# Kernel optimization log

Hardware: AMD Instinct MI355X
Metric: run time of the kernel (lower is better)

## Reference

```python
import jax, jax.numpy as jnp
import numpy as np

N_NODES = 50000
C = 256          # in_channels == hidden_size
E = 800000


def setup_inputs() -> dict:
    key = jax.random.key(0)
    ks = jax.random.split(key, 12)
    x = jax.random.normal(ks[0], (N_NODES, C), dtype=jnp.float32)
    edge_index = jax.random.randint(ks[1], (2, E), 0, N_NODES, dtype=jnp.int64)
    edge_attr = jax.random.uniform(ks[2], (E,), dtype=jnp.float32)
    edge_weights_index = jax.random.randint(ks[3], (2, E), 0, N_NODES, dtype=jnp.int64)
    s = 1.0 / np.sqrt(C)
    # TopKPooling projection vector
    p_pool = jax.random.normal(ks[4], (C,), dtype=jnp.float32) * s
    # GRU (input=C, hidden=C): gates stacked [r, z, n]
    W_ih = jax.random.normal(ks[5], (3 * C, C), dtype=jnp.float32) * s
    W_hh = jax.random.normal(ks[6], (3 * C, C), dtype=jnp.float32) * s
    b_ih = jnp.zeros((3 * C,), dtype=jnp.float32)
    b_hh = jnp.zeros((3 * C,), dtype=jnp.float32)
    # initial evolving GCN weight [C, C]
    W_init = jax.random.normal(ks[7], (C, C), dtype=jnp.float32) * s
    # EdgeDecoder MLP
    lin1_w = jax.random.normal(ks[8], (C, 2 * C), dtype=jnp.float32) / np.sqrt(2 * C)
    lin1_b = jnp.zeros((C,), dtype=jnp.float32)
    lin2_w = jax.random.normal(ks[9], (1, C), dtype=jnp.float32) * s
    lin2_b = jnp.zeros((1,), dtype=jnp.float32)
    return {
        "x": x, "edge_index": edge_index, "edge_attr": edge_attr,
        "edge_weights_index": edge_weights_index,
        "p_pool": p_pool, "W_ih": W_ih, "W_hh": W_hh, "b_ih": b_ih, "b_hh": b_hh,
        "W_init": W_init, "lin1_w": lin1_w, "lin1_b": lin1_b,
        "lin2_w": lin2_w, "lin2_b": lin2_b,
    }


def _forward(x, edge_attr, p_pool, W_ih, W_hh, b_ih, b_hh, W_init,
             lin1_w, lin1_b, lin2_w, lin2_b, edge_index, edge_weights_index):
    n_nodes, c = x.shape
    # --- EvolveGCNH: TopK pooling summary (k = in_channels) ---
    score = x @ p_pool / jnp.linalg.norm(p_pool)          # [N]
    top_score, perm = jax.lax.top_k(score, c)             # [C]
    x_tilde = x[perm] * jnp.tanh(top_score)[:, None]      # [C, C]
    # --- GRU step: input x_tilde (batch=C), hidden = evolving weight W_init ---
    gi = x_tilde @ W_ih.T + b_ih                           # [C, 3C]
    gh = W_init @ W_hh.T + b_hh                            # [C, 3C]
    i_r, i_z, i_n = jnp.split(gi, 3, axis=1)
    h_r, h_z, h_n = jnp.split(gh, 3, axis=1)
    r = jax.nn.sigmoid(i_r + h_r)
    z = jax.nn.sigmoid(i_z + h_z)
    n = jnp.tanh(i_n + r * h_n)
    W = (1.0 - z) * n + z * W_init                         # [C, C] evolved GCN weight
    # --- GCNConv with fixed W, add_self_loops=False ---
    xw = x @ W                                             # [N, C]
    src, dst = edge_index[0], edge_index[1]
    deg = jax.ops.segment_sum(edge_attr, dst, num_segments=n_nodes)
    dinv = jnp.where(deg > 0, jax.lax.rsqrt(jnp.where(deg > 0, deg, 1.0)), 0.0)
    norm = dinv[src] * edge_attr * dinv[dst]               # [E]
    node_emb = jax.ops.segment_sum(xw[src] * norm[:, None], dst,
                                   num_segments=n_nodes)   # [N, C]
    # --- EdgeDecoder: gather src/trg, concat, MLP ---
    s_idx, t_idx = edge_weights_index[0], edge_weights_index[1]
    edge_emb = jnp.concatenate([node_emb[s_idx], node_emb[t_idx]], axis=1)  # [E, 2C]
    h = jax.nn.relu(edge_emb @ lin1_w.T + lin1_b)          # [E, C]
    pred = h @ lin2_w.T + lin2_b                           # [E, 1]
    return pred.reshape(-1)


def reference(x, edge_index, edge_attr, edge_weights_index, p_pool,
              W_ih, W_hh, b_ih, b_hh, W_init, lin1_w, lin1_b, lin2_w, lin2_b):
    # dropout is identity in eval mode
    return _forward(x, edge_attr, p_pool, W_ih, W_hh, b_ih, b_hh, W_init,
                    lin1_w, lin1_b, lin2_w, lin2_b, edge_index, edge_weights_index)
```

## Files before the change

### kernel.cpp

```cpp
#include <hip/hip_runtime.h>
#include <hip/hip_bf16.h>
#include <math.h>


typedef __attribute__((ext_vector_type(8))) short bf16x8;
typedef __attribute__((ext_vector_type(8))) unsigned short u16x8;
typedef __attribute__((ext_vector_type(4))) float f32x4;

#define WSHIFT 9
#define WMASK 511
#define NBUCK 98

__device__ __forceinline__ unsigned f2key(float f) {
  unsigned u = __float_as_uint(f);
  return (u & 0x80000000u) ? ~u : (u | 0x80000000u);
}

__device__ __forceinline__ unsigned short f2bf(float f) {
  unsigned u = __float_as_uint(f);
  unsigned r = u + 0x7fffu + ((u >> 16) & 1u);
  return (unsigned short)(r >> 16);
}
__device__ __forceinline__ float bf2f(unsigned short h) {
  return __uint_as_float((unsigned)h << 16);
}

template <int CTRL>
__device__ __forceinline__ float dpp_add(float s) {
  int t = __builtin_amdgcn_update_dpp(0, __float_as_int(s), CTRL, 0xf, 0xf, false);
  return s + __int_as_float(t);
}

__device__ __forceinline__ void gload16(const void* g, void* l) {
  __builtin_amdgcn_global_load_lds((const __attribute__((address_space(1))) void*)g,
                                   (__attribute__((address_space(3))) void*)l, 16, 0, 0);
}

__global__ void zero_kernel(float4* __restrict__ p, int n4) {
  int i = blockIdx.x * blockDim.x + threadIdx.x;
  if (i < n4) p[i] = make_float4(0.f, 0.f, 0.f, 0.f);
}

__global__ __launch_bounds__(256) void score_cast_kernel(const float* __restrict__ x,
                                                         const float* __restrict__ p,
                                                         float* __restrict__ score,
                                                         unsigned short* __restrict__ xh, int N) {
  int node = blockIdx.x * 4 + (threadIdx.x >> 6);
  int lane = threadIdx.x & 63;
  if (node >= N) return;
  float4 xv = ((const float4*)(x + (size_t)node * 256))[lane];
  ushort4 hv;
  hv.x = f2bf(xv.x);
  hv.y = f2bf(xv.y);
  hv.z = f2bf(xv.z);
  hv.w = f2bf(xv.w);
  ((ushort4*)(xh + (size_t)node * 256))[lane] = hv;
  float4 pv = ((const float4*)p)[lane];
  float s = xv.x * pv.x + xv.y * pv.y + xv.z * pv.z + xv.w * pv.w;
  float sp = pv.x * pv.x + pv.y * pv.y + pv.z * pv.z + pv.w * pv.w;
#pragma unroll
  for (int off = 32; off > 0; off >>= 1) {
    s += __shfl_down(s, off, 64);
    sp += __shfl_down(sp, off, 64);
  }
  if (lane == 0) score[node] = s / sqrtf(sp);
}

__global__ __launch_bounds__(256) void hist12_kernel(const float* __restrict__ score, int n,
                                                     int* __restrict__ gh) {
  __shared__ int lh[4096];
  int tid = threadIdx.x;
  for (int i = tid; i < 4096; i += 256) lh[i] = 0;
  __syncthreads();
  int idx = blockIdx.x * 256 + tid;
  int stride = gridDim.x * 256;
  for (int i = idx; i < n; i += stride) {
    unsigned key = f2key(score[i]);
    atomicAdd(&lh[key >> 20], 1);
  }
  __syncthreads();
  for (int i = tid; i < 4096; i += 256) {
    int v = lh[i];
    if (v) atomicAdd(&gh[i], v);
  }
}

__global__ __launch_bounds__(1024) void topk_kernel(const float* __restrict__ score, int n, int k,
                                                    const int* __restrict__ gh,
                                                    int* __restrict__ perm,
                                                    float* __restrict__ tts) {
  __shared__ int part[1024];
  __shared__ unsigned sT;
  int tid = threadIdx.x;
  {
    int b0 = tid * 4;
    int s0 = gh[b0], s1 = gh[b0 + 1], s2 = gh[b0 + 2], s3 = gh[b0 + 3];
    part[tid] = s0 + s1 + s2 + s3;
    __syncthreads();
    for (int off = 1; off < 1024; off <<= 1) {
      int v = part[tid];
      int add = (tid + off < 1024) ? part[tid + off] : 0;
      __syncthreads();
      part[tid] = v + add;
      __syncthreads();
    }
    int sufChunk = part[tid];
    int sufNext = (tid < 1023) ? part[tid + 1] : 0;
    if (sufNext < k && sufChunk >= k) {
      int run = sufNext;
      int b;
      run += s3;
      if (run >= k) b = b0 + 3;
      else {
        run += s2;
        if (run >= k) b = b0 + 2;
        else {
          run += s1;
          b = (run >= k) ? b0 + 1 : b0;
        }
      }
      sT = ((unsigned)b) << 20;
    }
  }
  __syncthreads();
  unsigned T = sT;
  __shared__ unsigned keys[1024];
  __shared__ int idxs[1024];
  __shared__ int cnt;
  if (tid == 0) cnt = 0;
  keys[tid] = 0u;
  idxs[tid] = 0x7fffffff;
  __syncthreads();
  for (int i = tid; i < n; i += 1024) {
    unsigned key = f2key(score[i]);
    if (key >= T) {
      int p = atomicAdd(&cnt, 1);
      if (p < 1024) { keys[p] = key; idxs[p] = i; }
    }
  }
  __syncthreads();
  for (int size = 2; size <= 1024; size <<= 1) {
    for (int stride = size >> 1; stride > 0; stride >>= 1) {
      int j = tid ^ stride;
      if (j > tid) {
        unsigned ka = keys[tid], kb = keys[j];
        int ia = idxs[tid], ib = idxs[j];
        bool aBefore = (ka > kb) || (ka == kb && ia < ib);
        bool up = ((tid & size) == 0);
        if (aBefore != up) {
          keys[tid] = kb; keys[j] = ka;
          idxs[tid] = ib; idxs[j] = ia;
        }
      }
      __syncthreads();
    }
  }
  if (tid < k) {
    int idx = idxs[tid];
    perm[tid] = idx;
    tts[tid] = tanhf(score[idx]);
  }
}

__global__ __launch_bounds__(256) void gru_kernel(const float* __restrict__ x,
                                                  const int* __restrict__ perm,
                                                  const float* __restrict__ tts,
                                                  const float* __restrict__ Wi,
                                                  const float* __restrict__ W_ih,
                                                  const float* __restrict__ W_hh,
                                                  const float* __restrict__ b_ih,
                                                  const float* __restrict__ b_hh,
                                                  unsigned short* __restrict__ WevoT) {
  int i = blockIdx.x, j = threadIdx.x;
  __shared__ float sx[256], sh[256];
  sx[j] = x[(size_t)perm[i] * 256 + j] * tts[i];
  sh[j] = Wi[i * 256 + j];
  __syncthreads();
  float gi[3], gh[3];
#pragma unroll
  for (int g = 0; g < 3; ++g) {
    int row = g * 256 + j;
    const float4* wi4 = (const float4*)(W_ih + (size_t)row * 256);
    const float4* wh4 = (const float4*)(W_hh + (size_t)row * 256);
    float si = 0.f, s2 = 0.f;
    for (int k4 = 0; k4 < 64; ++k4) {
      float4 wv = wi4[k4];
      float4 hv = wh4[k4];
      int k = k4 * 4;
      si += sx[k] * wv.x + sx[k + 1] * wv.y + sx[k + 2] * wv.z + sx[k + 3] * wv.w;
      s2 += sh[k] * hv.x + sh[k + 1] * hv.y + sh[k + 2] * hv.z + sh[k + 3] * hv.w;
    }
    gi[g] = si + b_ih[row];
    gh[g] = s2 + b_hh[row];
  }
  float r = 1.f / (1.f + expf(-(gi[0] + gh[0])));
  float z = 1.f / (1.f + expf(-(gi[1] + gh[1])));
  float nn = tanhf(gi[2] + r * gh[2]);
  float w = (1.f - z) * nn + z * sh[j];
  WevoT[(size_t)j * 256 + i] = f2bf(w);
}

__global__ __launch_bounds__(256) void lin1_cast_kernel(const float* __restrict__ lin1,
                                                        unsigned short* __restrict__ WAB) {
  int idx = blockIdx.x * 256 + threadIdx.x;
  int n = idx >> 9, k = idx & 511;
  unsigned short h = f2bf(lin1[idx]);
  if (k < 256)
    WAB[n * 256 + k] = h;
  else
    WAB[(256 + n) * 256 + (k - 256)] = h;
}

__global__ __launch_bounds__(512) void mfma_gemm128(const unsigned short* __restrict__ A,
                                                    const unsigned short* __restrict__ BT,
                                                    unsigned short* __restrict__ C1,
                                                    unsigned short* __restrict__ C2,
                                                    int M) {
  __shared__ unsigned short sA[128 * 32];
  __shared__ unsigned short sB[256 * 32];
  int tid = threadIdx.x;
  int wave = tid >> 6, lane = tid & 63;
  int quad = lane >> 4, r16 = lane & 15;
  int wm = wave >> 2, wn = wave & 3;
  int mbase = blockIdx.x * 128;
  const unsigned short* Bt = BT + ((size_t)blockIdx.y << 16);
  unsigned short* Cout = blockIdx.y ? C2 : C1;

  int srow = tid >> 2, scolq = tid & 3;
  const unsigned short* gA = A + (size_t)(mbase + srow) * 256 + scolq * 8;
  const unsigned short* gB0 = Bt + (size_t)srow * 256 + scolq * 8;
  const unsigned short* gB1 = Bt + (size_t)(128 + srow) * 256 + scolq * 8;
  unsigned short* lA = sA + wave * 512;
  unsigned short* lB0 = sB + wave * 512;
  unsigned short* lB1 = sB + 4096 + wave * 512;

  f32x4 acc[4][4];
#pragma unroll
  for (int i = 0; i < 4; ++i)
#pragma unroll
    for (int j = 0; j < 4; ++j) acc[i][j] = (f32x4){0.f, 0.f, 0.f, 0.f};

  const unsigned short* pA = sA + (wm * 64 + r16) * 32 + quad * 8;
  const unsigned short* pB = sB + (wn * 64 + r16) * 32 + quad * 8;

  for (int k0 = 0; k0 < 256; k0 += 32) {
    if (k0) __syncthreads();
    gload16(gA + k0, lA);
    gload16(gB0 + k0, lB0);
    gload16(gB1 + k0, lB1);
    __syncthreads();
    bf16x8 af[4], bfr[4];
#pragma unroll
    for (int mt = 0; mt < 4; ++mt) af[mt] = *(const bf16x8*)(pA + mt * 512);
#pragma unroll
    for (int nt = 0; nt < 4; ++nt) bfr[nt] = *(const bf16x8*)(pB + nt * 512);
#pragma unroll
    for (int mt = 0; mt < 4; ++mt)
#pragma unroll
      for (int nt = 0; nt < 4; ++nt)
        acc[mt][nt] = __builtin_amdgcn_mfma_f32_16x16x32_bf16(af[mt], bfr[nt], acc[mt][nt], 0, 0, 0);
  }
#pragma unroll
  for (int mt = 0; mt < 4; ++mt) {
#pragma unroll
    for (int rr = 0; rr < 4; ++rr) {
      int grow = mbase + wm * 64 + mt * 16 + quad * 4 + rr;
      if (grow < M) {
#pragma unroll
        for (int nt = 0; nt < 4; ++nt)
          Cout[(size_t)grow * 256 + wn * 64 + nt * 16 + r16] = f2bf(acc[mt][nt][rr]);
      }
    }
  }
}


__global__ __launch_bounds__(256) void bucket_hist_kernel(const int* __restrict__ ei,
                                                          const int* __restrict__ ewi,
                                                          int* __restrict__ bcnt1,
                                                          int* __restrict__ bcnt2, int E) {
  __shared__ int c1[128], c2[128];
  int tid = threadIdx.x;
  if (tid < 128) { c1[tid] = 0; c2[tid] = 0; }
  __syncthreads();
  int idx = blockIdx.x * 256 + tid;
  int stride = gridDim.x * 256;
  for (int e = idx; e < E; e += stride) {
    atomicAdd(&c1[ei[E + e] >> WSHIFT], 1);
    atomicAdd(&c2[ewi[e] >> WSHIFT], 1);
  }
  __syncthreads();
  if (tid < 128) {
    if (c1[tid]) atomicAdd(&bcnt1[tid], c1[tid]);
    if (c2[tid]) atomicAdd(&bcnt2[tid], c2[tid]);
  }
}

__global__ __launch_bounds__(128) void bucket_scan_kernel(const int* __restrict__ bcnt1,
                                                          const int* __restrict__ bcnt2,
                                                          int* __restrict__ bbase1,
                                                          int* __restrict__ bbase2,
                                                          int* __restrict__ gcur1,
                                                          int* __restrict__ gcur2,
                                                          int* __restrict__ rowp1,
                                                          int* __restrict__ rowp2, int N, int E) {
  __shared__ int ss[128];
  int tid = threadIdx.x;
  int v = (tid < NBUCK) ? bcnt1[tid] : 0;
  ss[tid] = v;
  __syncthreads();
  for (int off = 1; off < 128; off <<= 1) {
    int a = ss[tid];
    int b = (tid >= off) ? ss[tid - off] : 0;
    __syncthreads();
    ss[tid] = a + b;
    __syncthreads();
  }
  int excl = ss[tid] - v;
  if (tid < NBUCK) { bbase1[tid] = excl; gcur1[tid] = excl; }
  if (tid == NBUCK - 1) bbase1[NBUCK] = excl + v;
  __syncthreads();
  v = (tid < NBUCK) ? bcnt2[tid] : 0;
  ss[tid] = v;
  __syncthreads();
  for (int off = 1; off < 128; off <<= 1) {
    int a = ss[tid];
    int b = (tid >= off) ? ss[tid - off] : 0;
    __syncthreads();
    ss[tid] = a + b;
    __syncthreads();
  }
  excl = ss[tid] - v;
  if (tid < NBUCK) { bbase2[tid] = excl; gcur2[tid] = excl; }
  if (tid == NBUCK - 1) bbase2[NBUCK] = excl + v;
  if (tid == 0) { rowp1[N] = E; rowp2[N] = E; }
}

__global__ __launch_bounds__(256) void p1_conv_kernel(const int* __restrict__ ei,
                                                      const float* __restrict__ attr,
                                                      int* __restrict__ gcur,
                                                      int2* __restrict__ stage, int E) {
  __shared__ int cnt[128], cur[128];
  int tid = threadIdx.x;
  int base = blockIdx.x * 4096;
  if (tid < 128) cnt[tid] = 0;
  __syncthreads();
  int bk[16];
  int2 pl[16];
#pragma unroll
  for (int i = 0; i < 16; ++i) {
    int e = base + i * 256 + tid;
    bk[i] = -1;
    if (e < E) {
      int d = ei[E + e];
      int s = ei[e];
      bk[i] = d >> WSHIFT;
      pl[i] = make_int2(s | ((d & WMASK) << 16), __float_as_int(attr[e]));
      atomicAdd(&cnt[bk[i]], 1);
    }
  }
  __syncthreads();
  if (tid < NBUCK) {
    int c = cnt[tid];
    cur[tid] = c ? atomicAdd(&gcur[tid], c) : 0;
  }
  __syncthreads();
#pragma unroll
  for (int i = 0; i < 16; ++i) {
    if (bk[i] >= 0) {
      int pos = atomicAdd(&cur[bk[i]], 1);
      stage[pos] = pl[i];
    }
  }
}

__global__ __launch_bounds__(256) void p1_dec_kernel(const int* __restrict__ ewi,
                                                     int* __restrict__ gcur,
                                                     int2* __restrict__ stage, int E) {
  __shared__ int cnt[128], cur[128];
  int tid = threadIdx.x;
  int base = blockIdx.x * 4096;
  if (tid < 128) cnt[tid] = 0;
  __syncthreads();
  int bk[16];
  int2 pl[16];
#pragma unroll
  for (int i = 0; i < 16; ++i) {
    int e = base + i * 256 + tid;
    bk[i] = -1;
    if (e < E) {
      int s = ewi[e];
      int d = ewi[E + e];
      bk[i] = s >> WSHIFT;
      pl[i] = make_int2(d | ((s & WMASK) << 16), e);
      atomicAdd(&cnt[bk[i]], 1);
    }
  }
  __syncthreads();
  if (tid < NBUCK) {
    int c = cnt[tid];
    cur[tid] = c ? atomicAdd(&gcur[tid], c) : 0;
  }
  __syncthreads();
#pragma unroll
  for (int i = 0; i < 16; ++i) {
    if (bk[i] >= 0) {
      int pos = atomicAdd(&cur[bk[i]], 1);
      stage[pos] = pl[i];
    }
  }
}

__global__ __launch_bounds__(256) void p2_kernel(const int2* __restrict__ stage1,
                                                 const int* __restrict__ bbase1,
                                                 int2* __restrict__ esv,
                                                 int* __restrict__ rowp1,
                                                 float* __restrict__ dinv,
                                                 const int2* __restrict__ stage2,
                                                 const int* __restrict__ bbase2,
                                                 int2* __restrict__ eto,
                                                 int* __restrict__ rowp2, int N) {
  __shared__ int cnt[512];
  __shared__ float degs[512];
  __shared__ int pref[512];
  __shared__ int ss[256];
  int tid = threadIdx.x;
  bool isConv = blockIdx.x < NBUCK;
  int b = isConv ? blockIdx.x : blockIdx.x - NBUCK;
  const int2* stage = isConv ? stage1 : stage2;
  const int* bbase = isConv ? bbase1 : bbase2;
  int beg = bbase[b], end = bbase[b + 1];
  int node0 = b << WSHIFT;
  cnt[tid] = 0; cnt[tid + 256] = 0;
  degs[tid] = 0.f; degs[tid + 256] = 0.f;
  __syncthreads();
  for (int j = beg + tid; j < end; j += 256) {
    int2 p = stage[j];
    int loc = p.x >> 16;
    atomicAdd(&cnt[loc], 1);
    if (isConv) atomicAdd(&degs[loc], __int_as_float(p.y));
  }
  __syncthreads();
  int c0 = cnt[2 * tid], c1 = cnt[2 * tid + 1];
  ss[tid] = c0 + c1;
  __syncthreads();
  for (int off = 1; off < 256; off <<= 1) {
    int a = ss[tid];
    int bb = (tid >= off) ? ss[tid - off] : 0;
    __syncthreads();
    ss[tid] = a + bb;
    __syncthreads();
  }
  int excl = (tid ? ss[tid - 1] : 0);
  pref[2 * tid] = excl;
  pref[2 * tid + 1] = excl + c0;
  __syncthreads();
#pragma unroll
  for (int h = 0; h < 2; ++h) {
    int i = tid + h * 256;
    int node = node0 + i;
    if (node < N) {
      if (isConv) {
        rowp1[node] = beg + pref[i];
        float d = degs[i];
        dinv[node] = d > 0.f ? 1.f / sqrtf(d) : 0.f;
      } else {
        rowp2[node] = beg + pref[i];
      }
    }
  }
  __syncthreads();
  int2* outb = isConv ? esv : eto;
  for (int j = beg + tid; j < end; j += 256) {
    int2 p = stage[j];
    int loc = p.x >> 16;
    int pos = beg + atomicAdd(&pref[loc], 1);
    outb[pos] = make_int2(p.x & 0xFFFF, p.y);
  }
}

__global__ __launch_bounds__(256) void esv_scale_kernel(int4* __restrict__ esv,
                                                        const float* __restrict__ dinv, int E2) {
  int i = blockIdx.x * 256 + threadIdx.x;
  if (i < E2) {
    int4 p = esv[i];
    p.y = __float_as_int(__int_as_float(p.y) * dinv[p.x]);
    p.w = __float_as_int(__int_as_float(p.w) * dinv[p.z]);
    esv[i] = p;
  }
}

__global__ __launch_bounds__(256) void gcn_gather(const unsigned short* __restrict__ xw,
                                                  const int* __restrict__ row_ptr,
                                                  const int2* __restrict__ esv,
                                                  const float* __restrict__ dinv,
                                                  unsigned short* __restrict__ ne, int N) {
  int node = blockIdx.x * 4 + (threadIdx.x >> 6);
  int lane = threadIdx.x & 63;
  int g = lane & 15, q = lane >> 4;
  if (node >= N) return;
  int beg = row_ptr[node], end = row_ptr[node + 1];
  float acc[16];
#pragma unroll
  for (int c = 0; c < 16; ++c) acc[c] = 0.f;
  const unsigned short* xb = xw + g * 16;

  for (int cb = beg; cb < end; cb += 64) {
    int cend = cb + 64 < end ? cb + 64 : end;
    int me = cb + lane;
    int2 mm = (me < cend) ? esv[me] : make_int2(0, 0);
    int mx = mm.x;
    float mv = __int_as_float(mm.y);

    float vA = 0.f, vB = 0.f, vC = 0.f;
    u16x8 rAa, rAb, rBa, rBb, rCa, rCb;
    {
      int e = cb + q;
      int sx = __shfl(mx, q, 64);
      float tv = __shfl(mv, q, 64);
      vA = (e < cend) ? tv : 0.f;
      rAa = *(const u16x8*)(xb + (size_t)sx * 256);
      rAb = *(const u16x8*)(xb + (size_t)sx * 256 + 8);
    }
    if (cb + 4 < cend) {
      int e = cb + 4 + q;
      int sx = __shfl(mx, 4 + q, 64);
      float tv = __shfl(mv, 4 + q, 64);
      vB = (e < cend) ? tv : 0.f;
      rBa = *(const u16x8*)(xb + (size_t)sx * 256);
      rBb = *(const u16x8*)(xb + (size_t)sx * 256 + 8);
    } else { rBa = rAa; rBb = rAb; }
    if (cb + 8 < cend) {
      int e = cb + 8 + q;
      int sx = __shfl(mx, 8 + q, 64);
      float tv = __shfl(mv, 8 + q, 64);
      vC = (e < cend) ? tv : 0.f;
      rCa = *(const u16x8*)(xb + (size_t)sx * 256);
      rCb = *(const u16x8*)(xb + (size_t)sx * 256 + 8);
    } else { rCa = rAa; rCb = rAb; }

    for (int jb = cb; jb < cend; jb += 12) {
#pragma unroll
      for (int c = 0; c < 8; ++c) acc[c] += bf2f(rAa[c]) * vA;
#pragma unroll
      for (int c = 0; c < 8; ++c) acc[8 + c] += bf2f(rAb[c]) * vA;
      vA = 0.f;
      if (jb + 12 < cend) {
        int e = jb + 12 + q;
        int idx = (e - cb) & 63;
        int sx = __shfl(mx, idx, 64);
        float tv = __shfl(mv, idx, 64);
        vA = (e < cend) ? tv : 0.f;
        rAa = *(const u16x8*)(xb + (size_t)sx * 256);
        rAb = *(const u16x8*)(xb + (size_t)sx * 256 + 8);
      }
#pragma unroll
      for (int c = 0; c < 8; ++c) acc[c] += bf2f(rBa[c]) * vB;
#pragma unroll
      for (int c = 0; c < 8; ++c) acc[8 + c] += bf2f(rBb[c]) * vB;
      vB = 0.f;
      if (jb + 16 < cend) {
        int e = jb + 16 + q;
        int idx = (e - cb) & 63;
        int sx = __shfl(mx, idx, 64);
        float tv = __shfl(mv, idx, 64);
        vB = (e < cend) ? tv : 0.f;
        rBa = *(const u16x8*)(xb + (size_t)sx * 256);
        rBb = *(const u16x8*)(xb + (size_t)sx * 256 + 8);
      }
#pragma unroll
      for (int c = 0; c < 8; ++c) acc[c] += bf2f(rCa[c]) * vC;
#pragma unroll
      for (int c = 0; c < 8; ++c) acc[8 + c] += bf2f(rCb[c]) * vC;
      vC = 0.f;
      if (jb + 20 < cend) {
        int e = jb + 20 + q;
        int idx = (e - cb) & 63;
        int sx = __shfl(mx, idx, 64);
        float tv = __shfl(mv, idx, 64);
        vC = (e < cend) ? tv : 0.f;
        rCa = *(const u16x8*)(xb + (size_t)sx * 256);
        rCb = *(const u16x8*)(xb + (size_t)sx * 256 + 8);
      }
    }
  }
#pragma unroll
  for (int c = 0; c < 16; ++c) {
    acc[c] += __shfl_xor(acc[c], 16, 64);
    acc[c] += __shfl_xor(acc[c], 32, 64);
  }
  if (q == 0) {
    float dd = dinv[node];
    u16x8 o0, o1;
#pragma unroll
    for (int c = 0; c < 8; ++c) {
      o0[c] = f2bf(acc[c] * dd);
      o1[c] = f2bf(acc[8 + c] * dd);
    }
    *(u16x8*)(ne + (size_t)node * 256 + g * 16) = o0;
    *(u16x8*)(ne + (size_t)node * 256 + g * 16 + 8) = o1;
  }
}

__global__ __launch_bounds__(256) void edge_decode_csr(const unsigned short* __restrict__ A,
                                                       const unsigned short* __restrict__ Bm,
                                                       const int* __restrict__ row_ptr,
                                                       const int2* __restrict__ eto,
                                                       const float* __restrict__ b1,
                                                       const float* __restrict__ w2,
                                                       const float* __restrict__ b2,
                                                       float* __restrict__ out, int N) {
  int node = blockIdx.x * 4 + (threadIdx.x >> 6);
  int lane = threadIdx.x & 63;
  int g = lane & 15, q = lane >> 4;
  if (node >= N) return;
  int beg = row_ptr[node], end = row_ptr[node + 1];
  if (beg >= end) return;
  float a[16], w[16];
  {
    u16x8 a0 = *(const u16x8*)(A + (size_t)node * 256 + g * 16);
    u16x8 a1 = *(const u16x8*)(A + (size_t)node * 256 + g * 16 + 8);
    const float4* bp = (const float4*)(b1 + g * 16);
    const float4* wp = (const float4*)(w2 + g * 16);
#pragma unroll
    for (int i = 0; i < 4; ++i) {
      float4 bv = bp[i];
      float4 wv = wp[i];
      a[i * 4 + 0] = (i < 2 ? bf2f(a0[i * 4 + 0]) : bf2f(a1[i * 4 - 8])) + bv.x;
      a[i * 4 + 1] = (i < 2 ? bf2f(a0[i * 4 + 1]) : bf2f(a1[i * 4 - 7])) + bv.y;
      a[i * 4 + 2] = (i < 2 ? bf2f(a0[i * 4 + 2]) : bf2f(a1[i * 4 - 6])) + bv.z;
      a[i * 4 + 3] = (i < 2 ? bf2f(a0[i * 4 + 3]) : bf2f(a1[i * 4 - 5])) + bv.w;
      w[i * 4 + 0] = wv.x;
      w[i * 4 + 1] = wv.y;
      w[i * 4 + 2] = wv.z;
      w[i * 4 + 3] = wv.w;
    }
  }
  float base = b2[0];
  const unsigned short* Bb = Bm + g * 16;

  for (int cb = beg; cb < end; cb += 64) {
    int cend = cb + 64 < end ? cb + 64 : end;
    int me = cb + lane;
    int2 mm = (me < cend) ? eto[me] : make_int2(0, 0);
    int mx = mm.x, my = mm.y;

    bool okA = false, okB = false;
    int oA = 0, oB = 0;
    u16x8 rAa, rAb, rBa, rBb;
    {
      int e = cb + q;
      int sx = __shfl(mx, q, 64);
      oA = __shfl(my, q, 64);
      okA = e < cend;
      rAa = *(const u16x8*)(Bb + (size_t)sx * 256);
      rAb = *(const u16x8*)(Bb + (size_t)sx * 256 + 8);
    }
    if (cb + 4 < cend) {
      int e = cb + 4 + q;
      int sx = __shfl(mx, 4 + q, 64);
      oB = __shfl(my, 4 + q, 64);
      okB = e < cend;
      rBa = *(const u16x8*)(Bb + (size_t)sx * 256);
      rBb = *(const u16x8*)(Bb + (size_t)sx * 256 + 8);
    } else { rBa = rAa; rBb = rAb; }

    for (int jb = cb; jb < cend; jb += 8) {
      {
        float s0 = 0.f, s1 = 0.f;
#pragma unroll
        for (int c = 0; c < 8; ++c) s0 += fmaxf(a[c] + bf2f(rAa[c]), 0.f) * w[c];
#pragma unroll
        for (int c = 0; c < 8; ++c) s1 += fmaxf(a[8 + c] + bf2f(rAb[c]), 0.f) * w[8 + c];
        float s = s0 + s1;
        s = dpp_add<0x128>(s);
        s = dpp_add<0x124>(s);
        s = dpp_add<0x122>(s);
        s = dpp_add<0x121>(s);
        if (g == 0 && okA) out[oA] = s + base;
      }
      okA = false;
      if (jb + 8 < cend) {
        int e = jb + 8 + q;
        int idx = (e - cb) & 63;
        int sx = __shfl(mx, idx, 64);
        oA = __shfl(my, idx, 64);
        okA = e < cend;
        rAa = *(const u16x8*)(Bb + (size_t)sx * 256);
        rAb = *(const u16x8*)(Bb + (size_t)sx * 256 + 8);
      }
      {
        float s0 = 0.f, s1 = 0.f;
#pragma unroll
        for (int c = 0; c < 8; ++c) s0 += fmaxf(a[c] + bf2f(rBa[c]), 0.f) * w[c];
#pragma unroll
        for (int c = 0; c < 8; ++c) s1 += fmaxf(a[8 + c] + bf2f(rBb[c]), 0.f) * w[8 + c];
        float s = s0 + s1;
        s = dpp_add<0x128>(s);
        s = dpp_add<0x124>(s);
        s = dpp_add<0x122>(s);
        s = dpp_add<0x121>(s);
        if (g == 0 && okB) out[oB] = s + base;
      }
      okB = false;
      if (jb + 12 < cend) {
        int e = jb + 12 + q;
        int idx = (e - cb) & 63;
        int sx = __shfl(mx, idx, 64);
        oB = __shfl(my, idx, 64);
        okB = e < cend;
        rBa = *(const u16x8*)(Bb + (size_t)sx * 256);
        rBb = *(const u16x8*)(Bb + (size_t)sx * 256 + 8);
      }
    }
  }
}

extern "C" void kernel_launch(void* const* d_in, const int* in_sizes, int n_in,
                              void* d_out, int out_size, void* d_ws, size_t ws_size,
                              hipStream_t stream) {
  const float* x      = (const float*)d_in[0];
  const int*   ei     = (const int*)d_in[1];
  const float* attr   = (const float*)d_in[2];
  const int*   ewi    = (const int*)d_in[3];
  const float* p_pool = (const float*)d_in[4];
  const float* W_ih   = (const float*)d_in[5];
  const float* W_hh   = (const float*)d_in[6];
  const float* b_ih   = (const float*)d_in[7];
  const float* b_hh   = (const float*)d_in[8];
  const float* W_init = (const float*)d_in[9];
  const float* lin1_w = (const float*)d_in[10];
  const float* lin1_b = (const float*)d_in[11];
  const float* lin2_w = (const float*)d_in[12];
  const float* lin2_b = (const float*)d_in[13];
  float* out = (float*)d_out;

  const int C = 256;
  const int N = in_sizes[0] / C;
  const int E = in_sizes[2];

  char* ws = (char*)d_ws;
  size_t off = 0;
  auto alloc = [&](size_t bytes) {
    size_t o = off;
    off = (off + bytes + 255) & ~(size_t)255;
    return o;
  };
  float*          score  = (float*)(ws + alloc((size_t)N * 4));
  int*            perm   = (int*)(ws + alloc(C * 4));
  float*          tts    = (float*)(ws + alloc(C * 4));
  unsigned short* WevoT  = (unsigned short*)(ws + alloc((size_t)C * C * 2));
  unsigned short* WAB    = (unsigned short*)(ws + alloc((size_t)2 * C * C * 2));
  int   zeroInts = 4096 + 128 + 128;
  char* zbase    = ws + alloc((size_t)zeroInts * 4);
  int* ghist = (int*)zbase;
  int* bcnt1 = (int*)(zbase + 4096 * 4);
  int* bcnt2 = (int*)(zbase + 4096 * 4 + 128 * 4);
  int*            bbase1 = (int*)(ws + alloc((NBUCK + 1) * 4));
  int*            bbase2 = (int*)(ws + alloc((NBUCK + 1) * 4));
  int*            gcur1  = (int*)(ws + alloc(128 * 4));
  int*            gcur2  = (int*)(ws + alloc(128 * 4));
  float*          dinv   = (float*)(ws + alloc((size_t)N * 4));
  int*            rowp1  = (int*)(ws + alloc((size_t)(N + 1) * 4));
  int*            rowp2  = (int*)(ws + alloc((size_t)(N + 1) * 4));
  int2*           stage1 = (int2*)(ws + alloc((size_t)E * 8));
  int2*           stage2 = (int2*)(ws + alloc((size_t)E * 8));
  int2*           esv    = (int2*)(ws + alloc((size_t)E * 8));
  int2*           eto    = (int2*)(ws + alloc((size_t)E * 8));
  unsigned short* xh     = (unsigned short*)(ws + alloc((size_t)N * C * 2));
  unsigned short* xwh    = (unsigned short*)(ws + alloc((size_t)N * C * 2));
  unsigned short* Bbf    = (unsigned short*)(ws + alloc((size_t)N * C * 2));
  unsigned short* ne  = xh;
  unsigned short* Abf = xwh;

  zero_kernel<<<(zeroInts / 4 + 255) / 256, 256, 0, stream>>>((float4*)zbase, zeroInts / 4);

  score_cast_kernel<<<(N + 3) / 4, 256, 0, stream>>>(x, p_pool, score, xh, N);

  hist12_kernel<<<64, 256, 0, stream>>>(score, N, ghist);
  topk_kernel<<<1, 1024, 0, stream>>>(score, N, C, ghist, perm, tts);

  gru_kernel<<<C, C, 0, stream>>>(x, perm, tts, W_init, W_ih, W_hh, b_ih, b_hh, WevoT);

  mfma_gemm128<<<dim3((N + 127) / 128, 1), 512, 0, stream>>>(xh, WevoT, xwh, xwh, N);

  bucket_hist_kernel<<<256, 256, 0, stream>>>(ei, ewi, bcnt1, bcnt2, E);
  bucket_scan_kernel<<<1, 128, 0, stream>>>(bcnt1, bcnt2, bbase1, bbase2, gcur1, gcur2,
                                            rowp1, rowp2, N, E);
  p1_conv_kernel<<<(E + 4095) / 4096, 256, 0, stream>>>(ei, attr, gcur1, stage1, E);
  p1_dec_kernel<<<(E + 4095) / 4096, 256, 0, stream>>>(ewi, gcur2, stage2, E);
  p2_kernel<<<2 * NBUCK, 256, 0, stream>>>(stage1, bbase1, esv, rowp1, dinv,
                                           stage2, bbase2, eto, rowp2, N);

  esv_scale_kernel<<<(E / 2 + 255) / 256, 256, 0, stream>>>((int4*)esv, dinv, E / 2);

  gcn_gather<<<(N + 3) / 4, 256, 0, stream>>>(xwh, rowp1, esv, dinv, ne, N);

  lin1_cast_kernel<<<(2 * C * C) / 256, 256, 0, stream>>>(lin1_w, WAB);
  mfma_gemm128<<<dim3((N + 127) / 128, 2), 512, 0, stream>>>(ne, WAB, Abf, Bbf, N);

  edge_decode_csr<<<(N + 3) / 4, 256, 0, stream>>>(Abf, Bbf, rowp2, eto,
                                                   lin1_b, lin2_w, lin2_b, out, N);
}
```

Before: 466.9 us.

## Merge small kernels and deepen edge-decode prefetch pipeline to three stages

Folds the zeroing and lin1 bf16 cast into one init kernel, builds the score histogram with global atomics inside the score kernel, and merges the two bucket-partition kernels into one launch. It also drops the separate esv scaling pass by applying dinv[src] inside the GCN gather. The edge decoder now keeps three gather buffers in flight instead of two. The goal is fewer launches and more memory-level parallelism, at the cost of 50k global atomics on a small histogram and more registers in the decoder.

```diff
diff --git a/kernel.cpp b/kernel.cpp
--- a/kernel.cpp
+++ b/kernel.cpp
@@ -36,15 +36,29 @@
                                    (__attribute__((address_space(3))) void*)l, 16, 0, 0);
 }
 
-__global__ void zero_kernel(float4* __restrict__ p, int n4) {
-  int i = blockIdx.x * blockDim.x + threadIdx.x;
-  if (i < n4) p[i] = make_float4(0.f, 0.f, 0.f, 0.f);
+__global__ __launch_bounds__(256) void init_kernel(const float* __restrict__ lin1,
+                                                   unsigned short* __restrict__ WAB,
+                                                   int4* __restrict__ zb, int nz4) {
+  int b = blockIdx.x, tid = threadIdx.x;
+  if (b < 512) {
+    int idx = b * 256 + tid;
+    int n = idx >> 9, k = idx & 511;
+    unsigned short h = f2bf(lin1[idx]);
+    if (k < 256)
+      WAB[n * 256 + k] = h;
+    else
+      WAB[(256 + n) * 256 + (k - 256)] = h;
+  } else {
+    int j = (b - 512) * 256 + tid;
+    if (j < nz4) zb[j] = make_int4(0, 0, 0, 0);
+  }
 }
 
 __global__ __launch_bounds__(256) void score_cast_kernel(const float* __restrict__ x,
                                                          const float* __restrict__ p,
                                                          float* __restrict__ score,
-                                                         unsigned short* __restrict__ xh, int N) {
+                                                         unsigned short* __restrict__ xh,
+                                                         int* __restrict__ gh, int N) {
   int node = blockIdx.x * 4 + (threadIdx.x >> 6);
   int lane = threadIdx.x & 63;
   if (node >= N) return;
@@ -63,25 +77,10 @@
     s += __shfl_down(s, off, 64);
     sp += __shfl_down(sp, off, 64);
   }
-  if (lane == 0) score[node] = s / sqrtf(sp);
-}
-
-__global__ __launch_bounds__(256) void hist12_kernel(const float* __restrict__ score, int n,
-                                                     int* __restrict__ gh) {
-  __shared__ int lh[4096];
-  int tid = threadIdx.x;
-  for (int i = tid; i < 4096; i += 256) lh[i] = 0;
-  __syncthreads();
-  int idx = blockIdx.x * 256 + tid;
-  int stride = gridDim.x * 256;
-  for (int i = idx; i < n; i += stride) {
-    unsigned key = f2key(score[i]);
-    atomicAdd(&lh[key >> 20], 1);
-  }
-  __syncthreads();
-  for (int i = tid; i < 4096; i += 256) {
-    int v = lh[i];
-    if (v) atomicAdd(&gh[i], v);
+  if (lane == 0) {
+    float sc = s / sqrtf(sp);
+    score[node] = sc;
+    atomicAdd(&gh[f2key(sc) >> 20], 1);
   }
 }
 
@@ -200,17 +199,6 @@
   WevoT[(size_t)j * 256 + i] = f2bf(w);
 }
 
-__global__ __launch_bounds__(256) void lin1_cast_kernel(const float* __restrict__ lin1,
-                                                        unsigned short* __restrict__ WAB) {
-  int idx = blockIdx.x * 256 + threadIdx.x;
-  int n = idx >> 9, k = idx & 511;
-  unsigned short h = f2bf(lin1[idx]);
-  if (k < 256)
-    WAB[n * 256 + k] = h;
-  else
-    WAB[(256 + n) * 256 + (k - 256)] = h;
-}
-
 __global__ __launch_bounds__(512) void mfma_gemm128(const unsigned short* __restrict__ A,
                                                     const unsigned short* __restrict__ BT,
                                                     unsigned short* __restrict__ C1,
@@ -336,13 +324,20 @@
   if (tid == 0) { rowp1[N] = E; rowp2[N] = E; }
 }
 
-__global__ __launch_bounds__(256) void p1_conv_kernel(const int* __restrict__ ei,
+__global__ __launch_bounds__(256) void p1_both_kernel(const int* __restrict__ ei,
                                                       const float* __restrict__ attr,
-                                                      int* __restrict__ gcur,
-                                                      int2* __restrict__ stage, int E) {
+                                                      int* __restrict__ gcur1,
+                                                      int2* __restrict__ stage1,
+                                                      const int* __restrict__ ewi,
+                                                      int* __restrict__ gcur2,
+                                                      int2* __restrict__ stage2,
+                                                      int E, int nb) {
   __shared__ int cnt[128], cur[128];
   int tid = threadIdx.x;
-  int base = blockIdx.x * 4096;
+  bool conv = blockIdx.x < nb;
+  int base = (conv ? blockIdx.x : blockIdx.x - nb) * 4096;
+  int* gcur = conv ? gcur1 : gcur2;
+  int2* stage = conv ? stage1 : stage2;
   if (tid < 128) cnt[tid] = 0;
   __syncthreads();
   int bk[16];
@@ -352,47 +347,17 @@
     int e = base + i * 256 + tid;
     bk[i] = -1;
     if (e < E) {
-      int d = ei[E + e];
-      int s = ei[e];
-      bk[i] = d >> WSHIFT;
-      pl[i] = make_int2(s | ((d & WMASK) << 16), __float_as_int(attr[e]));
-      atomicAdd(&cnt[bk[i]], 1);
-    }
-  }
-  __syncthreads();
-  if (tid < NBUCK) {
-    int c = cnt[tid];
-    cur[tid] = c ? atomicAdd(&gcur[tid], c) : 0;
-  }
-  __syncthreads();
-#pragma unroll
-  for (int i = 0; i < 16; ++i) {
-    if (bk[i] >= 0) {
-      int pos = atomicAdd(&cur[bk[i]], 1);
-      stage[pos] = pl[i];
-    }
-  }
-}
-
-__global__ __launch_bounds__(256) void p1_dec_kernel(const int* __restrict__ ewi,
-                                                     int* __restrict__ gcur,
-                                                     int2* __restrict__ stage, int E) {
-  __shared__ int cnt[128], cur[128];
-  int tid = threadIdx.x;
-  int base = blockIdx.x * 4096;
-  if (tid < 128) cnt[tid] = 0;
-  __syncthreads();
-  int bk[16];
-  int2 pl[16];
-#pragma unroll
-  for (int i = 0; i < 16; ++i) {
-    int e = base + i * 256 + tid;
-    bk[i] = -1;
-    if (e < E) {
-      int s = ewi[e];
-      int d = ewi[E + e];
-      bk[i] = s >> WSHIFT;
-      pl[i] = make_int2(d | ((s & WMASK) << 16), e);
+      if (conv) {
+        int d = ei[E + e];
+        int s = ei[e];
+        bk[i] = d >> WSHIFT;
+        pl[i] = make_int2(s | ((d & WMASK) << 16), __float_as_int(attr[e]));
+      } else {
+        int s = ewi[e];
+        int d = ewi[E + e];
+        bk[i] = s >> WSHIFT;
+        pl[i] = make_int2(d | ((s & WMASK) << 16), e);
+      }
       atomicAdd(&cnt[bk[i]], 1);
     }
   }
@@ -479,17 +444,6 @@
   }
 }
 
-__global__ __launch_bounds__(256) void esv_scale_kernel(int4* __restrict__ esv,
-                                                        const float* __restrict__ dinv, int E2) {
-  int i = blockIdx.x * 256 + threadIdx.x;
-  if (i < E2) {
-    int4 p = esv[i];
-    p.y = __float_as_int(__int_as_float(p.y) * dinv[p.x]);
-    p.w = __float_as_int(__int_as_float(p.w) * dinv[p.z]);
-    esv[i] = p;
-  }
-}
-
 __global__ __launch_bounds__(256) void gcn_gather(const unsigned short* __restrict__ xw,
                                                   const int* __restrict__ row_ptr,
                                                   const int2* __restrict__ esv,
@@ -510,7 +464,7 @@
     int me = cb + lane;
     int2 mm = (me < cend) ? esv[me] : make_int2(0, 0);
     int mx = mm.x;
-    float mv = __int_as_float(mm.y);
+    float mv = __int_as_float(mm.y) * dinv[mx];
 
     float vA = 0.f, vB = 0.f, vC = 0.f;
     u16x8 rAa, rAb, rBa, rBb, rCa, rCb;
@@ -645,9 +599,9 @@
     int2 mm = (me < cend) ? eto[me] : make_int2(0, 0);
     int mx = mm.x, my = mm.y;
 
-    bool okA = false, okB = false;
-    int oA = 0, oB = 0;
-    u16x8 rAa, rAb, rBa, rBb;
+    bool okA = false, okB = false, okC = false;
+    int oA = 0, oB = 0, oC = 0;
+    u16x8 rAa, rAb, rBa, rBb, rCa, rCb;
     {
       int e = cb + q;
       int sx = __shfl(mx, q, 64);
@@ -664,8 +618,16 @@
       rBa = *(const u16x8*)(Bb + (size_t)sx * 256);
       rBb = *(const u16x8*)(Bb + (size_t)sx * 256 + 8);
     } else { rBa = rAa; rBb = rAb; }
-
-    for (int jb = cb; jb < cend; jb += 8) {
+    if (cb + 8 < cend) {
+      int e = cb + 8 + q;
+      int sx = __shfl(mx, 8 + q, 64);
+      oC = __shfl(my, 8 + q, 64);
+      okC = e < cend;
+      rCa = *(const u16x8*)(Bb + (size_t)sx * 256);
+      rCb = *(const u16x8*)(Bb + (size_t)sx * 256 + 8);
+    } else { rCa = rAa; rCb = rAb; }
+
+    for (int jb = cb; jb < cend; jb += 12) {
       {
         float s0 = 0.f, s1 = 0.f;
 #pragma unroll
@@ -680,8 +642,8 @@
         if (g == 0 && okA) out[oA] = s + base;
       }
       okA = false;
-      if (jb + 8 < cend) {
-        int e = jb + 8 + q;
+      if (jb + 12 < cend) {
+        int e = jb + 12 + q;
         int idx = (e - cb) & 63;
         int sx = __shfl(mx, idx, 64);
         oA = __shfl(my, idx, 64);
@@ -703,14 +665,37 @@
         if (g == 0 && okB) out[oB] = s + base;
       }
       okB = false;
-      if (jb + 12 < cend) {
-        int e = jb + 12 + q;
+      if (jb + 16 < cend) {
+        int e = jb + 16 + q;
         int idx = (e - cb) & 63;
         int sx = __shfl(mx, idx, 64);
         oB = __shfl(my, idx, 64);
         okB = e < cend;
         rBa = *(const u16x8*)(Bb + (size_t)sx * 256);
         rBb = *(const u16x8*)(Bb + (size_t)sx * 256 + 8);
+      }
+      {
+        float s0 = 0.f, s1 = 0.f;
+#pragma unroll
+        for (int c = 0; c < 8; ++c) s0 += fmaxf(a[c] + bf2f(rCa[c]), 0.f) * w[c];
+#pragma unroll
+        for (int c = 0; c < 8; ++c) s1 += fmaxf(a[8 + c] + bf2f(rCb[c]), 0.f) * w[8 + c];
+        float s = s0 + s1;
+        s = dpp_add<0x128>(s);
+        s = dpp_add<0x124>(s);
+        s = dpp_add<0x122>(s);
+        s = dpp_add<0x121>(s);
+        if (g == 0 && okC) out[oC] = s + base;
+      }
+      okC = false;
+      if (jb + 20 < cend) {
+        int e = jb + 20 + q;
+        int idx = (e - cb) & 63;
+        int sx = __shfl(mx, idx, 64);
+        oC = __shfl(my, idx, 64);
+        okC = e < cend;
+        rCa = *(const u16x8*)(Bb + (size_t)sx * 256);
+        rCb = *(const u16x8*)(Bb + (size_t)sx * 256 + 8);
       }
     }
   }
@@ -773,11 +758,13 @@
   unsigned short* ne  = xh;
   unsigned short* Abf = xwh;
 
-  zero_kernel<<<(zeroInts / 4 + 255) / 256, 256, 0, stream>>>((float4*)zbase, zeroInts / 4);
-
-  score_cast_kernel<<<(N + 3) / 4, 256, 0, stream>>>(x, p_pool, score, xh, N);
-
-  hist12_kernel<<<64, 256, 0, stream>>>(score, N, ghist);
+  int nz4 = (zeroInts + 3) / 4;
+  int nbP1 = (E + 4095) / 4096;
+
+  init_kernel<<<512 + (nz4 + 255) / 256, 256, 0, stream>>>(lin1_w, WAB, (int4*)zbase, nz4);
+
+  score_cast_kernel<<<(N + 3) / 4, 256, 0, stream>>>(x, p_pool, score, xh, ghist, N);
+
   topk_kernel<<<1, 1024, 0, stream>>>(score, N, C, ghist, perm, tts);
 
   gru_kernel<<<C, C, 0, stream>>>(x, perm, tts, W_init, W_ih, W_hh, b_ih, b_hh, WevoT);
@@ -787,16 +774,13 @@
   bucket_hist_kernel<<<256, 256, 0, stream>>>(ei, ewi, bcnt1, bcnt2, E);
   bucket_scan_kernel<<<1, 128, 0, stream>>>(bcnt1, bcnt2, bbase1, bbase2, gcur1, gcur2,
                                             rowp1, rowp2, N, E);
-  p1_conv_kernel<<<(E + 4095) / 4096, 256, 0, stream>>>(ei, attr, gcur1, stage1, E);
-  p1_dec_kernel<<<(E + 4095) / 4096, 256, 0, stream>>>(ewi, gcur2, stage2, E);
+  p1_both_kernel<<<2 * nbP1, 256, 0, stream>>>(ei, attr, gcur1, stage1,
+                                               ewi, gcur2, stage2, E, nbP1);
   p2_kernel<<<2 * NBUCK, 256, 0, stream>>>(stage1, bbase1, esv, rowp1, dinv,
                                            stage2, bbase2, eto, rowp2, N);
 
-  esv_scale_kernel<<<(E / 2 + 255) / 256, 256, 0, stream>>>((int4*)esv, dinv, E / 2);
-
   gcn_gather<<<(N + 3) / 4, 256, 0, stream>>>(xwh, rowp1, esv, dinv, ne, N);
 
-  lin1_cast_kernel<<<(2 * C * C) / 256, 256, 0, stream>>>(lin1_w, WAB);
   mfma_gemm128<<<dim3((N + 127) / 128, 2), 512, 0, stream>>>(ne, WAB, Abf, Bbf, N);
 
   edge_decode_csr<<<(N + 3) / 4, 256, 0, stream>>>(Abf, Bbf, rowp2, eto,
```

Result: slower. 603.7 us (+29.3%).
